# Optimization experiments

Measured on AMD Instinct MI355X. Metric: run time of the kernel, lower is better.

Reference implementation:

```python
import jax, jax.numpy as jnp
import numpy as np

B, S, DIM = 2, 2048, 2048
NH, NKV = 32, 8
HD = DIM // NH  # 64


def setup_inputs() -> dict:
    key = jax.random.key(0)
    ks = jax.random.split(key, 6)
    x = jax.random.normal(ks[0], (B, S, DIM), jnp.float32)
    # realistic rotary tables: [S, HD//2]
    inv_freq = 1.0 / (10000.0 ** (jnp.arange(0, HD, 2, dtype=jnp.float32) / HD))
    freqs = jnp.arange(S, dtype=jnp.float32)[:, None] * inv_freq[None, :]
    cos, sin = jnp.cos(freqs), jnp.sin(freqs)
    init = lambda k, shape: jax.random.normal(k, shape, jnp.float32) * (shape[0] ** -0.5)
    Wq = init(ks[1], (DIM, NH * HD))
    Wk = init(ks[2], (DIM, NKV * HD))
    Wv = init(ks[3], (DIM, NKV * HD))
    Wo = init(ks[4], (NH * HD, DIM))
    return {"x": x, "cos": cos, "sin": sin, "Wq": Wq, "Wk": Wk, "Wv": Wv, "Wo": Wo}


def _rope(t, c, s):
    # t: [B, S, H, HD]; c, s: [1, S, 1, HD//2]; consecutive-pair (v1) style
    b, sl, h, hd = t.shape
    tp = t.reshape(b, sl, h, hd // 2, 2)
    t0, t1 = tp[..., 0], tp[..., 1]
    return jnp.stack([t0 * c - t1 * s, t0 * s + t1 * c], axis=-1).reshape(b, sl, h, hd)


def reference(x, cos, sin, Wq, Wk, Wv, Wo):
    b, sl, _ = x.shape
    q = (x @ Wq).reshape(b, sl, NH, HD)
    k = (x @ Wk).reshape(b, sl, NKV, HD)
    v = (x @ Wv).reshape(b, sl, NKV, HD)
    c = cos[None, :, None, :]
    s = sin[None, :, None, :]
    q = _rope(q, c, s)
    k = _rope(k, c, s)
    n_rep = NH // NKV
    k = jnp.repeat(k, n_rep, axis=2)  # GQA repeat_interleave over heads
    v = jnp.repeat(v, n_rep, axis=2)
    scale = 1.0 / np.sqrt(HD)
    scores = jnp.einsum("bqhd,bkhd->bhqk", q, k) * scale  # [B, H, S, S]
    causal = jnp.tril(jnp.ones((sl, sl), dtype=bool))
    scores = jnp.where(causal[None, None], scores, -jnp.inf)
    p = jax.nn.softmax(scores, axis=-1)
    out = jnp.einsum("bhqk,bkhd->bqhd", p, v).reshape(b, sl, NH * HD)
    return out @ Wo
```

## Files before the change

### kernel.cpp

```cpp
#include <hip/hip_runtime.h>
#include <hip/hip_bf16.h>


typedef __attribute__((ext_vector_type(8))) short short8;
typedef __attribute__((ext_vector_type(4))) float f32x4;
typedef __attribute__((ext_vector_type(16))) float f32x16;
typedef __attribute__((ext_vector_type(2))) int i32x2;
typedef __attribute__((ext_vector_type(4))) int i32x4;

__device__ __forceinline__ unsigned short f2bfu(float f){
  unsigned u = __float_as_uint(f);
  u += 0x7FFFu + ((u >> 16) & 1u);
  return (unsigned short)(u >> 16);
}
__device__ __forceinline__ float bfu2f(unsigned short u){
  return __uint_as_float(((unsigned)u) << 16);
}
__device__ __forceinline__ unsigned cvt_pk_bf16(float lo, float hi){
  unsigned r;
  asm("v_cvt_pk_bf16_f32 %0, %1, %2" : "=v"(r) : "v"(lo), "v"(hi));
  return r;
}
__device__ __forceinline__ i32x2 pl32swap(int a, int b){
  auto r = __builtin_amdgcn_permlane32_swap(a, b, false, false);
  return __builtin_bit_cast(i32x2, r);
}
__device__ __forceinline__ int swz64(int row, int slot){
  return row * 64 + (((slot) ^ (row & 7)) << 3);
}
template<int N> __device__ __forceinline__ void vm_wait(){
  if constexpr (N == 8)      asm volatile("s_waitcnt vmcnt(8)" ::: "memory");
  else if constexpr (N == 7) asm volatile("s_waitcnt vmcnt(7)" ::: "memory");
  else if constexpr (N == 6) asm volatile("s_waitcnt vmcnt(6)" ::: "memory");
  else if constexpr (N == 4) asm volatile("s_waitcnt vmcnt(4)" ::: "memory");
  else if constexpr (N == 3) asm volatile("s_waitcnt vmcnt(3)" ::: "memory");
  else if constexpr (N == 2) asm volatile("s_waitcnt vmcnt(2)" ::: "memory");
  else                       asm volatile("s_waitcnt vmcnt(0)" ::: "memory");
}

__global__ void convx_kernel(const float* __restrict__ x, unsigned short* __restrict__ xb, int n4){
  int i = blockIdx.x * blockDim.x + threadIdx.x;
  if (i >= n4) return;
  float4 v = reinterpret_cast<const float4*>(x)[i];
  ushort4 o;
  o.x = f2bfu(v.x); o.y = f2bfu(v.y); o.z = f2bfu(v.z); o.w = f2bfu(v.w);
  reinterpret_cast<ushort4*>(xb)[i] = o;
}

__global__ void transpose_conv_kernel(const float* __restrict__ in, unsigned short* __restrict__ out,
                                      int Min, int Nin){
  __shared__ float t[32][33];
  int c0 = blockIdx.x * 32, r0 = blockIdx.y * 32;
  int tx = threadIdx.x, ty = threadIdx.y;
  #pragma unroll
  for (int i = ty; i < 32; i += 8) t[i][tx] = in[(size_t)(r0 + i) * Nin + c0 + tx];
  __syncthreads();
  #pragma unroll
  for (int i = ty; i < 32; i += 8) out[(size_t)(c0 + i) * Min + r0 + tx] = f2bfu(t[tx][i]);
}

#define PH4(SLOT,KK,VMW,...) { \
  const unsigned short* sAc = &sA[SLOT][(KK)*8192]; \
  const unsigned short* sBc = &sB[SLOT][(KK)*RB]; \
  short8 afr[8]; short8 bfr[4]; \
  _Pragma("unroll") for (int m_ = 0; m_ < 8; m_++) \
    afr[m_] = *reinterpret_cast<const short8*>(sAc + aOff[m_]); \
  _Pragma("unroll") for (int n_ = 0; n_ < NF; n_++) \
    bfr[n_] = *reinterpret_cast<const short8*>(sBc + bOff[n_]); \
  __VA_ARGS__; \
  __builtin_amdgcn_s_barrier(); \
  asm volatile("s_waitcnt lgkmcnt(0)" ::: "memory"); \
  __builtin_amdgcn_sched_barrier(0); \
  __builtin_amdgcn_s_setprio(1); \
  _Pragma("unroll") for (int m_ = 0; m_ < 8; m_++){ \
    _Pragma("unroll") for (int n_ = 0; n_ < NF; n_++){ \
      acc[m_][n_] = __builtin_amdgcn_mfma_f32_16x16x32_bf16(afr[m_], bfr[n_], acc[m_][n_], 0, 0, 0); }} \
  __builtin_amdgcn_s_setprio(0); \
  VMW; \
  __builtin_amdgcn_s_barrier(); \
}

template<int NF, bool OUTBF16>
__global__ __launch_bounds__(512, 2) void gemm4p_kernel(const unsigned short* __restrict__ A,
                                                        const unsigned short* __restrict__ B,
                                                        void* __restrict__ Cp,
                                                        int M, int N, int K, int nbx){
  constexpr int RB  = NF * 2048;
  constexpr int VMS = (NF == 4) ? 8 : (NF == 3 ? 7 : 6);
  __shared__ unsigned short sA[2][16384];
  __shared__ unsigned short sB[2][2 * RB];
  const int tid = threadIdx.x;
  const int l = tid & 63, w = tid >> 6;
  const int quad = l >> 4, c16 = l & 15;
  const int cpx = (int)gridDim.x >> 3;
  const int id2 = ((int)blockIdx.x & 7) * cpx + ((int)blockIdx.x >> 3);
  const int bx = id2 % nbx, by = id2 / nbx;
  const int row0 = by * 256, col0 = bx * (NF * 64);
  const int wr = w >> 2, wc = w & 3;

  const int rlA0 = w * 32 + (l >> 2), rlA1 = rlA0 + 16;
  const unsigned short* gA0 = A + (size_t)(row0 + rlA0) * K + (((l & 3) ^ ((rlA0 >> 1) & 3)) << 3);
  const unsigned short* gA1 = A + (size_t)(row0 + rlA1) * K + (((l & 3) ^ ((rlA1 >> 1) & 3)) << 3);
  const unsigned short* gB0;
  const unsigned short* gB1 = nullptr;
  const unsigned short* gB2 = nullptr;
  if constexpr (NF == 4){
    gB0 = B + (size_t)(col0 + rlA0) * K + (((l & 3) ^ ((rlA0 >> 1) & 3)) << 3);
    gB1 = B + (size_t)(col0 + rlA1) * K + (((l & 3) ^ ((rlA1 >> 1) & 3)) << 3);
  } else {
    const int rlB0 = w * 16 + (l >> 2);
    gB0 = B + (size_t)(col0 + rlB0) * K + (((l & 3) ^ ((rlB0 >> 1) & 3)) << 3);
    if constexpr (NF == 3){
      const int rlB2 = 128 + (w & 3) * 16 + (l >> 2);
      gB2 = B + (size_t)(col0 + rlB2) * K + (((l & 3) ^ ((rlB2 >> 1) & 3)) << 3);
    }
  }

  auto stA = [&](int slot, int kk, int col){
    __builtin_amdgcn_global_load_lds((const __attribute__((address_space(1))) void*)(gA0 + col),
        (__attribute__((address_space(3))) void*)(&sA[slot][kk * 8192 + w * 1024]), 16, 0, 0);
    __builtin_amdgcn_global_load_lds((const __attribute__((address_space(1))) void*)(gA1 + col),
        (__attribute__((address_space(3))) void*)(&sA[slot][kk * 8192 + w * 1024 + 512]), 16, 0, 0);
  };
  auto stB = [&](int slot, int kk, int col){
    if constexpr (NF == 4){
      __builtin_amdgcn_global_load_lds((const __attribute__((address_space(1))) void*)(gB0 + col),
          (__attribute__((address_space(3))) void*)(&sB[slot][kk * RB + w * 1024]), 16, 0, 0);
      __builtin_amdgcn_global_load_lds((const __attribute__((address_space(1))) void*)(gB1 + col),
          (__attribute__((address_space(3))) void*)(&sB[slot][kk * RB + w * 1024 + 512]), 16, 0, 0);
    } else if constexpr (NF == 3){
      __builtin_amdgcn_global_load_lds((const __attribute__((address_space(1))) void*)(gB0 + col),
          (__attribute__((address_space(3))) void*)(&sB[slot][kk * RB + w * 512]), 16, 0, 0);
      if ((kk == 0) ? (w < 4) : (w >= 4))
        __builtin_amdgcn_global_load_lds((const __attribute__((address_space(1))) void*)(gB2 + col),
            (__attribute__((address_space(3))) void*)(&sB[slot][kk * RB + 4096 + (w & 3) * 512]), 16, 0, 0);
    } else {
      __builtin_amdgcn_global_load_lds((const __attribute__((address_space(1))) void*)(gB0 + col),
          (__attribute__((address_space(3))) void*)(&sB[slot][kk * RB + w * 512]), 16, 0, 0);
    }
  };

  int aOff[8], bOff[4];
  #pragma unroll
  for (int mf = 0; mf < 8; mf++){
    int row = wr * 128 + mf * 16 + c16;
    aOff[mf] = row * 32 + ((quad ^ ((row >> 1) & 3)) << 3);
  }
  #pragma unroll
  for (int nf = 0; nf < 4; nf++){
    int row = wc * (NF * 16) + nf * 16 + c16;
    bOff[nf] = row * 32 + ((quad ^ ((row >> 1) & 3)) << 3);
  }

  stA(0, 0, 0);  stB(0, 0, 0);
  stA(0, 1, 32); stB(0, 1, 32);
  stA(1, 0, 64); stB(1, 0, 64);
  vm_wait<VMS>();
  __builtin_amdgcn_s_barrier();

  f32x4 acc[8][4] = {};
  const int NI = K >> 7;
  #pragma unroll 1
  for (int j = 0; j < NI - 1; ++j){
    const int t1c  = (2 * j + 1) * 64 + 32;
    const int t2c0 = (2 * j + 2) * 64;
    const int t2c1 = t2c0 + 32;
    const int t3c0 = (2 * j + 3) * 64;
    PH4(0,0, vm_wait<VMS>(), stA(1,1,t1c);  stB(1,1,t1c))
    PH4(0,1, vm_wait<VMS>(), stA(0,0,t2c0); stB(0,0,t2c0))
    PH4(1,0, vm_wait<VMS>(), stA(0,1,t2c1); stB(0,1,t2c1))
    PH4(1,1, vm_wait<VMS>(), stA(1,0,t3c0); stB(1,0,t3c0))
  }
  {
    const int t1c = K - 32;
    PH4(0,0, vm_wait<VMS>(), stA(1,1,t1c); stB(1,1,t1c))
    PH4(0,1, vm_wait<0>(), ;)
    PH4(1,0, vm_wait<0>(), ;)
    PH4(1,1, (void)0, ;)
  }

  #pragma unroll
  for (int mf = 0; mf < 8; mf++)
    #pragma unroll
    for (int nf = 0; nf < NF; nf++)
      #pragma unroll
      for (int r = 0; r < 4; r++){
        size_t off = (size_t)(row0 + wr * 128 + mf * 16 + quad * 4 + r) * N + (col0 + wc * (NF * 16) + nf * 16 + c16);
        if (OUTBF16) ((unsigned short*)Cp)[off] = f2bfu(acc[mf][nf][r]);
        else         ((float*)Cp)[off] = acc[mf][nf][r];
      }
}

__global__ void rope_kernel(const unsigned short* __restrict__ qkv, const float* __restrict__ cosb,
                            const float* __restrict__ sinb, unsigned short* __restrict__ Qo,
                            unsigned short* __restrict__ Ko){
  int idx = blockIdx.x * 256 + threadIdx.x;
  const int NQ = 4096 * 1024;
  if (idx < NQ){
    int m = idx >> 10, p = idx & 1023;
    int h = p >> 5, i = p & 31;
    int s = m & 2047;
    unsigned pr = *reinterpret_cast<const unsigned*>(qkv + (size_t)m * 3072 + h * 64 + 2 * i);
    float t0 = bfu2f((unsigned short)(pr & 0xFFFFu));
    float t1 = bfu2f((unsigned short)(pr >> 16));
    float c = cosb[s * 32 + i], sn = sinb[s * 32 + i];
    const float SC = 0.18033688011112042f;
    float o0 = (t0 * c - t1 * sn) * SC;
    float o1 = (t0 * sn + t1 * c) * SC;
    unsigned ow = (unsigned)f2bfu(o0) | ((unsigned)f2bfu(o1) << 16);
    *reinterpret_cast<unsigned*>(Qo + (size_t)m * 2048 + h * 64 + 2 * i) = ow;
  } else {
    int j = idx - NQ;
    int m = j >> 8, p = j & 255;
    int kvh = p >> 5, i = p & 31;
    int s = m & 2047, b = m >> 11;
    unsigned pr = *reinterpret_cast<const unsigned*>(qkv + (size_t)m * 3072 + 2048 + kvh * 64 + 2 * i);
    float t0 = bfu2f((unsigned short)(pr & 0xFFFFu));
    float t1 = bfu2f((unsigned short)(pr >> 16));
    float c = cosb[s * 32 + i], sn = sinb[s * 32 + i];
    float o0 = t0 * c - t1 * sn;
    float o1 = t0 * sn + t1 * c;
    unsigned ow = (unsigned)f2bfu(o0) | ((unsigned)f2bfu(o1) << 16);
    *reinterpret_cast<unsigned*>(Ko + ((size_t)(b * 8 + kvh) * 2048 + s) * 64 + 2 * i) = ow;
  }
}

__global__ void vtrans_kernel(const unsigned short* __restrict__ qkv, unsigned short* __restrict__ Vt){
  __shared__ float t[64][65];
  int bh = blockIdx.y;
  int s0 = blockIdx.x * 64;
  int b = bh >> 3, kvh = bh & 7;
  int tid = threadIdx.x;
  #pragma unroll
  for (int it = 0; it < 16; it++){
    int id = it * 256 + tid;
    int sl = id >> 6, d = id & 63;
    unsigned short u = qkv[(size_t)(b * 2048 + s0 + sl) * 3072 + 2560 + kvh * 64 + d];
    t[sl][d] = bfu2f(u);
  }
  __syncthreads();
  #pragma unroll
  for (int it = 0; it < 16; it++){
    int id = it * 256 + tid;
    int dl = id >> 6, sl = id & 63;
    Vt[((size_t)(b * 8 + kvh) * 64 + dl) * 2048 + s0 + sl] = f2bfu(t[sl][dl]);
  }
}

__global__ __launch_bounds__(256) void attn_kernel(const unsigned short* __restrict__ Q,
                                                   const unsigned short* __restrict__ Kt,
                                                   const unsigned short* __restrict__ Vt,
                                                   unsigned short* __restrict__ O){
  __shared__ unsigned short sK[2][64 * 64];
  __shared__ unsigned short sV[2][64 * 64];
  const int tid = threadIdx.x;
  const int l = tid & 63, w = tid >> 6;
  const int q32 = l & 31, hi = l >> 5;
  const int bid = blockIdx.x;
  const int qt = 15 - (bid >> 6);
  const int bh = bid & 63;
  const int b = bh >> 5, h = bh & 31, kvh = h >> 2;
  const int q0w = qt * 128 + w * 32;
  const int nt = 2 * qt + 2;

  const unsigned short* Kb = Kt + (size_t)(b * 8 + kvh) * 2048 * 64;
  const unsigned short* Vb = Vt + (size_t)(b * 8 + kvh) * 64 * 2048;

  auto stage = [&](int kv0, int buf){
    #pragma unroll
    for (int c = 0; c < 2; c++){
      const int rl = w * 16 + c * 8 + (l >> 3);
      const int ce = (((l & 7) ^ (l >> 3)) << 3);
      __builtin_amdgcn_global_load_lds(
        (const __attribute__((address_space(1))) void*)(Kb + (size_t)(kv0 + rl) * 64 + ce),
        (__attribute__((address_space(3))) void*)(&sK[buf][(w * 16 + c * 8) * 64]), 16, 0, 0);
      __builtin_amdgcn_global_load_lds(
        (const __attribute__((address_space(1))) void*)(Vb + (size_t)rl * 2048 + kv0 + ce),
        (__attribute__((address_space(3))) void*)(&sV[buf][(w * 16 + c * 8) * 64]), 16, 0, 0);
    }
  };

  short8 qv[4];
  {
    const unsigned short* Qp = Q + (size_t)(b * 2048 + q0w + q32) * 2048 + h * 64 + hi * 8;
    #pragma unroll
    for (int kd = 0; kd < 4; kd++) qv[kd] = *reinterpret_cast<const short8*>(Qp + kd * 16);
  }

  const short8 ones = {0x3F80, 0x3F80, 0x3F80, 0x3F80, 0x3F80, 0x3F80, 0x3F80, 0x3F80};

  f32x16 accA = {}, accB = {};
  f32x16 accl = {};

#define MKAP(Z, R0, AP) { \
    unsigned A_ = cvt_pk_bf16(Z[R0+0], Z[R0+1]); \
    unsigned B_ = cvt_pk_bf16(Z[R0+2], Z[R0+3]); \
    unsigned C_ = cvt_pk_bf16(Z[R0+4], Z[R0+5]); \
    unsigned D_ = cvt_pk_bf16(Z[R0+6], Z[R0+7]); \
    i32x2 s1_ = pl32swap((int)A_, (int)C_); \
    i32x2 s2_ = pl32swap((int)B_, (int)D_); \
    i32x4 q_ = {s1_[0], s2_[0], s1_[1], s2_[1]}; \
    AP = __builtin_bit_cast(short8, q_); \
  }

  stage(0, 0);
  vm_wait<0>();
  __builtin_amdgcn_s_barrier();

  for (int t = 0; t < nt; ++t){
    const int kv0 = t * 64;
    const int buf = t & 1;
    if (t + 1 < nt) stage((t + 1) * 64, buf ^ 1);

    const unsigned short* sKc = &sK[buf][0];
    const unsigned short* sVc = &sV[buf][0];

    f32x16 z0 = {}, z1 = {};
    __builtin_amdgcn_s_setprio(1);
    #pragma unroll
    for (int kd = 0; kd < 4; kd++){
      const int u = kd * 2 + hi;
      short8 ak0 = *reinterpret_cast<const short8*>(&sKc[swz64(q32, u)]);
      short8 ak1 = *reinterpret_cast<const short8*>(&sKc[swz64(32 + q32, u)]);
      z0 = __builtin_amdgcn_mfma_f32_32x32x16_bf16(ak0, qv[kd], z0, 0, 0, 0);
      z1 = __builtin_amdgcn_mfma_f32_32x32x16_bf16(ak1, qv[kd], z1, 0, 0, 0);
    }
    __builtin_amdgcn_s_setprio(0);

    if (kv0 + 63 > q0w){
      const int qg = q0w + q32;
      #pragma unroll
      for (int r = 0; r < 16; r++){
        const int kr = (r & 3) + 8 * (r >> 2) + 4 * hi;
        if (kv0 + kr > qg)      z0[r] = -1e30f;
        if (kv0 + 32 + kr > qg) z1[r] = -1e30f;
      }
    }

    #pragma unroll
    for (int r = 0; r < 16; r++){
      z0[r] = __builtin_amdgcn_exp2f(z0[r]);
      z1[r] = __builtin_amdgcn_exp2f(z1[r]);
    }

    short8 apA, apB;
    __builtin_amdgcn_s_setprio(1);
    MKAP(z0, 0, apA)
    MKAP(z0, 8, apB)
    accl = __builtin_amdgcn_mfma_f32_32x32x16_bf16(apA, ones, accl, 0, 0, 0);
    accl = __builtin_amdgcn_mfma_f32_32x32x16_bf16(apB, ones, accl, 0, 0, 0);
    {
      short8 bv;
      bv = *reinterpret_cast<const short8*>(&sVc[swz64(q32, 0 * 2 + hi)]);
      accA = __builtin_amdgcn_mfma_f32_32x32x16_bf16(apA, bv, accA, 0, 0, 0);
      bv = *reinterpret_cast<const short8*>(&sVc[swz64(q32, 1 * 2 + hi)]);
      accA = __builtin_amdgcn_mfma_f32_32x32x16_bf16(apB, bv, accA, 0, 0, 0);
      bv = *reinterpret_cast<const short8*>(&sVc[swz64(32 + q32, 0 * 2 + hi)]);
      accB = __builtin_amdgcn_mfma_f32_32x32x16_bf16(apA, bv, accB, 0, 0, 0);
      bv = *reinterpret_cast<const short8*>(&sVc[swz64(32 + q32, 1 * 2 + hi)]);
      accB = __builtin_amdgcn_mfma_f32_32x32x16_bf16(apB, bv, accB, 0, 0, 0);
    }
    MKAP(z1, 0, apA)
    MKAP(z1, 8, apB)
    accl = __builtin_amdgcn_mfma_f32_32x32x16_bf16(apA, ones, accl, 0, 0, 0);
    accl = __builtin_amdgcn_mfma_f32_32x32x16_bf16(apB, ones, accl, 0, 0, 0);
    {
      short8 bv;
      bv = *reinterpret_cast<const short8*>(&sVc[swz64(q32, 2 * 2 + hi)]);
      accA = __builtin_amdgcn_mfma_f32_32x32x16_bf16(apA, bv, accA, 0, 0, 0);
      bv = *reinterpret_cast<const short8*>(&sVc[swz64(q32, 3 * 2 + hi)]);
      accA = __builtin_amdgcn_mfma_f32_32x32x16_bf16(apB, bv, accA, 0, 0, 0);
      bv = *reinterpret_cast<const short8*>(&sVc[swz64(32 + q32, 2 * 2 + hi)]);
      accB = __builtin_amdgcn_mfma_f32_32x32x16_bf16(apA, bv, accB, 0, 0, 0);
      bv = *reinterpret_cast<const short8*>(&sVc[swz64(32 + q32, 3 * 2 + hi)]);
      accB = __builtin_amdgcn_mfma_f32_32x32x16_bf16(apB, bv, accB, 0, 0, 0);
    }
    __builtin_amdgcn_s_setprio(0);

    vm_wait<0>();
    __builtin_amdgcn_s_barrier();
  }
#undef MKAP

  #pragma unroll
  for (int r = 0; r < 16; r++){
    const float inv = 1.0f / accl[r];
    const int qrow = q0w + (r & 3) + 8 * (r >> 2) + 4 * hi;
    const size_t base = (size_t)(b * 2048 + qrow) * 2048 + h * 64 + q32;
    O[base]      = f2bfu(accA[r] * inv);
    O[base + 32] = f2bfu(accB[r] * inv);
  }
}

extern "C" void kernel_launch(void* const* d_in, const int* in_sizes, int n_in,
                              void* d_out, int out_size, void* d_ws, size_t ws_size,
                              hipStream_t stream){
  (void)in_sizes; (void)n_in; (void)out_size; (void)ws_size;
  const float* x  = (const float*)d_in[0];
  const float* cb = (const float*)d_in[1];
  const float* sb = (const float*)d_in[2];
  const float* Wq = (const float*)d_in[3];
  const float* Wk = (const float*)d_in[4];
  const float* Wv = (const float*)d_in[5];
  const float* Wo = (const float*)d_in[6];
  float* out = (float*)d_out;
  char* ws = (char*)d_ws;

  unsigned short* qkv = (unsigned short*)(ws + 0);
  unsigned short* xb  = (unsigned short*)(ws + 25165824);
  unsigned short* wt  = (unsigned short*)(ws + 41943040);
  unsigned short* qb  = (unsigned short*)(ws + 54525952);
  unsigned short* kb  = (unsigned short*)(ws + 71303168);
  unsigned short* vt  = (unsigned short*)(ws + 75497472);

  dim3 tb(32, 8);
  convx_kernel<<<8192, 256, 0, stream>>>(x, xb, 2097152);
  transpose_conv_kernel<<<dim3(64, 64), tb, 0, stream>>>(Wq, wt, 2048, 2048);
  transpose_conv_kernel<<<dim3(16, 64), tb, 0, stream>>>(Wk, wt + (size_t)2048 * 2048, 2048, 512);
  transpose_conv_kernel<<<dim3(16, 64), tb, 0, stream>>>(Wv, wt + (size_t)2560 * 2048, 2048, 512);
  gemm4p_kernel<3, true><<<256, 512, 0, stream>>>(xb, wt, qkv, 4096, 3072, 2048, 16);
  rope_kernel<<<20480, 256, 0, stream>>>(qkv, cb, sb, qb, kb);
  vtrans_kernel<<<dim3(32, 16), 256, 0, stream>>>(qkv, vt);
  transpose_conv_kernel<<<dim3(64, 64), tb, 0, stream>>>(Wo, wt, 2048, 2048);
  attn_kernel<<<1024, 256, 0, stream>>>(qb, kb, vt, xb);
  gemm4p_kernel<2, false><<<256, 512, 0, stream>>>(xb, wt, out, 4096, 2048, 2048, 16);
}
```

Baseline: 194.8 us.

## Double-buffer GEMM LDS fragments in registers to overlap reads with MFMA

The bf16 GEMM main loop now loads the next phase's A/B fragments from shared memory into a second register buffer while MFMAs run on the current fragments. This removes the pre-compute barrier and the LDS-latency stall at the start of each phase. A prologue preloads the first fragments and an epilogue macro handles the last compute. The global-load wait count is retuned for the new schedule. The second fragment buffer raises register pressure under the 512-thread, 2-block launch bounds, which risks spills or lower occupancy.

After: 196.0 us. No clear change (+0.6%).

```diff
diff --git a/kernel.cpp b/kernel.cpp
--- a/kernel.cpp
+++ b/kernel.cpp
@@ -59,25 +59,30 @@
   for (int i = ty; i < 32; i += 8) out[(size_t)(c0 + i) * Min + r0 + tx] = f2bfu(t[tx][i]);
 }
 
-#define PH4(SLOT,KK,VMW,...) { \
-  const unsigned short* sAc = &sA[SLOT][(KK)*8192]; \
-  const unsigned short* sBc = &sB[SLOT][(KK)*RB]; \
-  short8 afr[8]; short8 bfr[4]; \
+#define PH4P(NS,NK,CUR,NXT,VMW,...) { \
+  const unsigned short* sAn = &sA[NS][(NK)*8192]; \
+  const unsigned short* sBn = &sB[NS][(NK)*RB]; \
   _Pragma("unroll") for (int m_ = 0; m_ < 8; m_++) \
-    afr[m_] = *reinterpret_cast<const short8*>(sAc + aOff[m_]); \
+    afr[NXT][m_] = *reinterpret_cast<const short8*>(sAn + aOff[m_]); \
   _Pragma("unroll") for (int n_ = 0; n_ < NF; n_++) \
-    bfr[n_] = *reinterpret_cast<const short8*>(sBc + bOff[n_]); \
+    bfr[NXT][n_] = *reinterpret_cast<const short8*>(sBn + bOff[n_]); \
   __VA_ARGS__; \
-  __builtin_amdgcn_s_barrier(); \
-  asm volatile("s_waitcnt lgkmcnt(0)" ::: "memory"); \
   __builtin_amdgcn_sched_barrier(0); \
   __builtin_amdgcn_s_setprio(1); \
   _Pragma("unroll") for (int m_ = 0; m_ < 8; m_++){ \
     _Pragma("unroll") for (int n_ = 0; n_ < NF; n_++){ \
-      acc[m_][n_] = __builtin_amdgcn_mfma_f32_16x16x32_bf16(afr[m_], bfr[n_], acc[m_][n_], 0, 0, 0); }} \
+      acc[m_][n_] = __builtin_amdgcn_mfma_f32_16x16x32_bf16(afr[CUR][m_], bfr[CUR][n_], acc[m_][n_], 0, 0, 0); }} \
   __builtin_amdgcn_s_setprio(0); \
+  asm volatile("s_waitcnt lgkmcnt(0)" ::: "memory"); \
   VMW; \
   __builtin_amdgcn_s_barrier(); \
+}
+#define PH4L(CUR) { \
+  __builtin_amdgcn_s_setprio(1); \
+  _Pragma("unroll") for (int m_ = 0; m_ < 8; m_++){ \
+    _Pragma("unroll") for (int n_ = 0; n_ < NF; n_++){ \
+      acc[m_][n_] = __builtin_amdgcn_mfma_f32_16x16x32_bf16(afr[CUR][m_], bfr[CUR][n_], acc[m_][n_], 0, 0, 0); }} \
+  __builtin_amdgcn_s_setprio(0); \
 }
 
 template<int NF, bool OUTBF16>
@@ -85,8 +90,8 @@
                                                         const unsigned short* __restrict__ B,
                                                         void* __restrict__ Cp,
                                                         int M, int N, int K, int nbx){
-  constexpr int RB  = NF * 2048;
-  constexpr int VMS = (NF == 4) ? 8 : (NF == 3 ? 7 : 6);
+  constexpr int RB   = NF * 2048;
+  constexpr int VMS2 = (NF == 4) ? 4 : 3;
   __shared__ unsigned short sA[2][16384];
   __shared__ unsigned short sB[2][2 * RB];
   const int tid = threadIdx.x;
@@ -155,10 +160,17 @@
   stA(0, 0, 0);  stB(0, 0, 0);
   stA(0, 1, 32); stB(0, 1, 32);
   stA(1, 0, 64); stB(1, 0, 64);
-  vm_wait<VMS>();
+  vm_wait<VMS2>();
   __builtin_amdgcn_s_barrier();
 
   f32x4 acc[8][4] = {};
+  short8 afr[2][8];
+  short8 bfr[2][4];
+  #pragma unroll
+  for (int m_ = 0; m_ < 8; m_++) afr[0][m_] = *reinterpret_cast<const short8*>(&sA[0][0] + aOff[m_]);
+  #pragma unroll
+  for (int n_ = 0; n_ < NF; n_++) bfr[0][n_] = *reinterpret_cast<const short8*>(&sB[0][0] + bOff[n_]);
+
   const int NI = K >> 7;
   #pragma unroll 1
   for (int j = 0; j < NI - 1; ++j){
@@ -166,17 +178,17 @@
     const int t2c0 = (2 * j + 2) * 64;
     const int t2c1 = t2c0 + 32;
     const int t3c0 = (2 * j + 3) * 64;
-    PH4(0,0, vm_wait<VMS>(), stA(1,1,t1c);  stB(1,1,t1c))
-    PH4(0,1, vm_wait<VMS>(), stA(0,0,t2c0); stB(0,0,t2c0))
-    PH4(1,0, vm_wait<VMS>(), stA(0,1,t2c1); stB(0,1,t2c1))
-    PH4(1,1, vm_wait<VMS>(), stA(1,0,t3c0); stB(1,0,t3c0))
+    PH4P(0,1, 0,1, vm_wait<VMS2>(), stA(1,1,t1c);  stB(1,1,t1c))
+    PH4P(1,0, 1,0, vm_wait<VMS2>(), stA(0,0,t2c0); stB(0,0,t2c0))
+    PH4P(1,1, 0,1, vm_wait<VMS2>(), stA(0,1,t2c1); stB(0,1,t2c1))
+    PH4P(0,0, 1,0, vm_wait<VMS2>(), stA(1,0,t3c0); stB(1,0,t3c0))
   }
   {
     const int t1c = K - 32;
-    PH4(0,0, vm_wait<VMS>(), stA(1,1,t1c); stB(1,1,t1c))
-    PH4(0,1, vm_wait<0>(), ;)
-    PH4(1,0, vm_wait<0>(), ;)
-    PH4(1,1, (void)0, ;)
+    PH4P(0,1, 0,1, vm_wait<VMS2>(), stA(1,1,t1c); stB(1,1,t1c))
+    PH4P(1,0, 1,0, vm_wait<0>(), ;)
+    PH4P(1,1, 0,1, (void)0, ;)
+    PH4L(1)
   }
 
   #pragma unroll
```

## Retile GEMM to 128-row blocks with 4 waves and larger per-wave N tiles

Applied to the files above, without the earlier changes.

Shrinks the GEMM block tile from 256 rows with 8 waves to 128 rows with 4 waves (2x2 wave grid), each wave computing 64 rows by 2*NF*16 columns. The grid doubles to 512 blocks, which changes wave quantisation across CUs, and LDS use per block drops. The global-to-LDS load mapping is generalised and the vmcnt thresholds are rescaled to match. Each block now loads more B data relative to its A tile, which lowers arithmetic intensity per block.

Measured after the change: 193.3 us. About the same (-0.8%).

```diff
diff --git a/kernel.cpp b/kernel.cpp
--- a/kernel.cpp
+++ b/kernel.cpp
@@ -29,13 +29,15 @@
   return row * 64 + (((slot) ^ (row & 7)) << 3);
 }
 template<int N> __device__ __forceinline__ void vm_wait(){
-  if constexpr (N == 8)      asm volatile("s_waitcnt vmcnt(8)" ::: "memory");
-  else if constexpr (N == 7) asm volatile("s_waitcnt vmcnt(7)" ::: "memory");
-  else if constexpr (N == 6) asm volatile("s_waitcnt vmcnt(6)" ::: "memory");
-  else if constexpr (N == 4) asm volatile("s_waitcnt vmcnt(4)" ::: "memory");
-  else if constexpr (N == 3) asm volatile("s_waitcnt vmcnt(3)" ::: "memory");
-  else if constexpr (N == 2) asm volatile("s_waitcnt vmcnt(2)" ::: "memory");
-  else                       asm volatile("s_waitcnt vmcnt(0)" ::: "memory");
+  if constexpr (N == 10)      asm volatile("s_waitcnt vmcnt(10)" ::: "memory");
+  else if constexpr (N == 8)  asm volatile("s_waitcnt vmcnt(8)" ::: "memory");
+  else if constexpr (N == 7)  asm volatile("s_waitcnt vmcnt(7)" ::: "memory");
+  else if constexpr (N == 6)  asm volatile("s_waitcnt vmcnt(6)" ::: "memory");
+  else if constexpr (N == 5)  asm volatile("s_waitcnt vmcnt(5)" ::: "memory");
+  else if constexpr (N == 4)  asm volatile("s_waitcnt vmcnt(4)" ::: "memory");
+  else if constexpr (N == 3)  asm volatile("s_waitcnt vmcnt(3)" ::: "memory");
+  else if constexpr (N == 2)  asm volatile("s_waitcnt vmcnt(2)" ::: "memory");
+  else                        asm volatile("s_waitcnt vmcnt(0)" ::: "memory");
 }
 
 __global__ void convx_kernel(const float* __restrict__ x, unsigned short* __restrict__ xb, int n4){
@@ -60,20 +62,20 @@
 }
 
 #define PH4(SLOT,KK,VMW,...) { \
-  const unsigned short* sAc = &sA[SLOT][(KK)*8192]; \
+  const unsigned short* sAc = &sA[SLOT][(KK)*4096]; \
   const unsigned short* sBc = &sB[SLOT][(KK)*RB]; \
-  short8 afr[8]; short8 bfr[4]; \
-  _Pragma("unroll") for (int m_ = 0; m_ < 8; m_++) \
+  short8 afr[4]; short8 bfr[6]; \
+  _Pragma("unroll") for (int m_ = 0; m_ < 4; m_++) \
     afr[m_] = *reinterpret_cast<const short8*>(sAc + aOff[m_]); \
-  _Pragma("unroll") for (int n_ = 0; n_ < NF; n_++) \
+  _Pragma("unroll") for (int n_ = 0; n_ < NFR; n_++) \
     bfr[n_] = *reinterpret_cast<const short8*>(sBc + bOff[n_]); \
   __VA_ARGS__; \
   __builtin_amdgcn_s_barrier(); \
   asm volatile("s_waitcnt lgkmcnt(0)" ::: "memory"); \
   __builtin_amdgcn_sched_barrier(0); \
   __builtin_amdgcn_s_setprio(1); \
-  _Pragma("unroll") for (int m_ = 0; m_ < 8; m_++){ \
-    _Pragma("unroll") for (int n_ = 0; n_ < NF; n_++){ \
+  _Pragma("unroll") for (int m_ = 0; m_ < 4; m_++){ \
+    _Pragma("unroll") for (int n_ = 0; n_ < NFR; n_++){ \
       acc[m_][n_] = __builtin_amdgcn_mfma_f32_16x16x32_bf16(afr[m_], bfr[n_], acc[m_][n_], 0, 0, 0); }} \
   __builtin_amdgcn_s_setprio(0); \
   VMW; \
@@ -81,13 +83,14 @@
 }
 
 template<int NF, bool OUTBF16>
-__global__ __launch_bounds__(512, 2) void gemm4p_kernel(const unsigned short* __restrict__ A,
+__global__ __launch_bounds__(256, 2) void gemm4p_kernel(const unsigned short* __restrict__ A,
                                                         const unsigned short* __restrict__ B,
                                                         void* __restrict__ Cp,
                                                         int M, int N, int K, int nbx){
+  constexpr int NFR = 2 * NF;
   constexpr int RB  = NF * 2048;
-  constexpr int VMS = (NF == 4) ? 8 : (NF == 3 ? 7 : 6);
-  __shared__ unsigned short sA[2][16384];
+  constexpr int VMS = 2 * (2 + NF);
+  __shared__ unsigned short sA[2][8192];
   __shared__ unsigned short sB[2][2 * RB];
   const int tid = threadIdx.x;
   const int l = tid & 63, w = tid >> 6;
@@ -95,60 +98,44 @@
   const int cpx = (int)gridDim.x >> 3;
   const int id2 = ((int)blockIdx.x & 7) * cpx + ((int)blockIdx.x >> 3);
   const int bx = id2 % nbx, by = id2 / nbx;
-  const int row0 = by * 256, col0 = bx * (NF * 64);
-  const int wr = w >> 2, wc = w & 3;
-
-  const int rlA0 = w * 32 + (l >> 2), rlA1 = rlA0 + 16;
-  const unsigned short* gA0 = A + (size_t)(row0 + rlA0) * K + (((l & 3) ^ ((rlA0 >> 1) & 3)) << 3);
-  const unsigned short* gA1 = A + (size_t)(row0 + rlA1) * K + (((l & 3) ^ ((rlA1 >> 1) & 3)) << 3);
-  const unsigned short* gB0;
-  const unsigned short* gB1 = nullptr;
-  const unsigned short* gB2 = nullptr;
-  if constexpr (NF == 4){
-    gB0 = B + (size_t)(col0 + rlA0) * K + (((l & 3) ^ ((rlA0 >> 1) & 3)) << 3);
-    gB1 = B + (size_t)(col0 + rlA1) * K + (((l & 3) ^ ((rlA1 >> 1) & 3)) << 3);
-  } else {
-    const int rlB0 = w * 16 + (l >> 2);
-    gB0 = B + (size_t)(col0 + rlB0) * K + (((l & 3) ^ ((rlB0 >> 1) & 3)) << 3);
-    if constexpr (NF == 3){
-      const int rlB2 = 128 + (w & 3) * 16 + (l >> 2);
-      gB2 = B + (size_t)(col0 + rlB2) * K + (((l & 3) ^ ((rlB2 >> 1) & 3)) << 3);
-    }
+  const int row0 = by * 128, col0 = bx * (NF * 64);
+  const int wr = w >> 1, wc = w & 1;
+
+  const unsigned short* gAp[2];
+  const unsigned short* gBp[NF];
+  #pragma unroll
+  for (int j = 0; j < 2; j++){
+    int rl = w * 32 + j * 16 + (l >> 2);
+    gAp[j] = A + (size_t)(row0 + rl) * K + ((((l & 3) ^ ((rl >> 1) & 3))) << 3);
+  }
+  #pragma unroll
+  for (int j = 0; j < NF; j++){
+    int rl = w * (16 * NF) + j * 16 + (l >> 2);
+    gBp[j] = B + (size_t)(col0 + rl) * K + ((((l & 3) ^ ((rl >> 1) & 3))) << 3);
   }
 
   auto stA = [&](int slot, int kk, int col){
-    __builtin_amdgcn_global_load_lds((const __attribute__((address_space(1))) void*)(gA0 + col),
-        (__attribute__((address_space(3))) void*)(&sA[slot][kk * 8192 + w * 1024]), 16, 0, 0);
-    __builtin_amdgcn_global_load_lds((const __attribute__((address_space(1))) void*)(gA1 + col),
-        (__attribute__((address_space(3))) void*)(&sA[slot][kk * 8192 + w * 1024 + 512]), 16, 0, 0);
+    #pragma unroll
+    for (int j = 0; j < 2; j++)
+      __builtin_amdgcn_global_load_lds((const __attribute__((address_space(1))) void*)(gAp[j] + col),
+          (__attribute__((address_space(3))) void*)(&sA[slot][kk * 4096 + w * 1024 + j * 512]), 16, 0, 0);
   };
   auto stB = [&](int slot, int kk, int col){
-    if constexpr (NF == 4){
-      __builtin_amdgcn_global_load_lds((const __attribute__((address_space(1))) void*)(gB0 + col),
-          (__attribute__((address_space(3))) void*)(&sB[slot][kk * RB + w * 1024]), 16, 0, 0);
-      __builtin_amdgcn_global_load_lds((const __attribute__((address_space(1))) void*)(gB1 + col),
-          (__attribute__((address_space(3))) void*)(&sB[slot][kk * RB + w * 1024 + 512]), 16, 0, 0);
-    } else if constexpr (NF == 3){
-      __builtin_amdgcn_global_load_lds((const __attribute__((address_space(1))) void*)(gB0 + col),
-          (__attribute__((address_space(3))) void*)(&sB[slot][kk * RB + w * 512]), 16, 0, 0);
-      if ((kk == 0) ? (w < 4) : (w >= 4))
-        __builtin_amdgcn_global_load_lds((const __attribute__((address_space(1))) void*)(gB2 + col),
-            (__attribute__((address_space(3))) void*)(&sB[slot][kk * RB + 4096 + (w & 3) * 512]), 16, 0, 0);
-    } else {
-      __builtin_amdgcn_global_load_lds((const __attribute__((address_space(1))) void*)(gB0 + col),
-          (__attribute__((address_space(3))) void*)(&sB[slot][kk * RB + w * 512]), 16, 0, 0);
-    }
+    #pragma unroll
+    for (int j = 0; j < NF; j++)
+      __builtin_amdgcn_global_load_lds((const __attribute__((address_space(1))) void*)(gBp[j] + col),
+          (__attribute__((address_space(3))) void*)(&sB[slot][kk * RB + w * (512 * NF) + j * 512]), 16, 0, 0);
   };
 
-  int aOff[8], bOff[4];
-  #pragma unroll
-  for (int mf = 0; mf < 8; mf++){
-    int row = wr * 128 + mf * 16 + c16;
+  int aOff[4], bOff[6];
+  #pragma unroll
+  for (int mf = 0; mf < 4; mf++){
+    int row = wr * 64 + mf * 16 + c16;
     aOff[mf] = row * 32 + ((quad ^ ((row >> 1) & 3)) << 3);
   }
   #pragma unroll
-  for (int nf = 0; nf < 4; nf++){
-    int row = wc * (NF * 16) + nf * 16 + c16;
+  for (int nf = 0; nf < NFR; nf++){
+    int row = wc * (NF * 32) + nf * 16 + c16;
     bOff[nf] = row * 32 + ((quad ^ ((row >> 1) & 3)) << 3);
   }
 
@@ -158,7 +145,7 @@
   vm_wait<VMS>();
   __builtin_amdgcn_s_barrier();
 
-  f32x4 acc[8][4] = {};
+  f32x4 acc[4][6] = {};
   const int NI = K >> 7;
   #pragma unroll 1
   for (int j = 0; j < NI - 1; ++j){
@@ -180,12 +167,12 @@
   }
 
   #pragma unroll
-  for (int mf = 0; mf < 8; mf++)
-    #pragma unroll
-    for (int nf = 0; nf < NF; nf++)
+  for (int mf = 0; mf < 4; mf++)
+    #pragma unroll
+    for (int nf = 0; nf < NFR; nf++)
       #pragma unroll
       for (int r = 0; r < 4; r++){
-        size_t off = (size_t)(row0 + wr * 128 + mf * 16 + quad * 4 + r) * N + (col0 + wc * (NF * 16) + nf * 16 + c16);
+        size_t off = (size_t)(row0 + wr * 64 + mf * 16 + quad * 4 + r) * N + (col0 + wc * (NF * 32) + nf * 16 + c16);
         if (OUTBF16) ((unsigned short*)Cp)[off] = f2bfu(acc[mf][nf][r]);
         else         ((float*)Cp)[off] = acc[mf][nf][r];
       }
@@ -418,10 +405,10 @@
   transpose_conv_kernel<<<dim3(64, 64), tb, 0, stream>>>(Wq, wt, 2048, 2048);
   transpose_conv_kernel<<<dim3(16, 64), tb, 0, stream>>>(Wk, wt + (size_t)2048 * 2048, 2048, 512);
   transpose_conv_kernel<<<dim3(16, 64), tb, 0, stream>>>(Wv, wt + (size_t)2560 * 2048, 2048, 512);
-  gemm4p_kernel<3, true><<<256, 512, 0, stream>>>(xb, wt, qkv, 4096, 3072, 2048, 16);
+  gemm4p_kernel<3, true><<<512, 256, 0, stream>>>(xb, wt, qkv, 4096, 3072, 2048, 16);
   rope_kernel<<<20480, 256, 0, stream>>>(qkv, cb, sb, qb, kb);
   vtrans_kernel<<<dim3(32, 16), 256, 0, stream>>>(qkv, vt);
   transpose_conv_kernel<<<dim3(64, 64), tb, 0, stream>>>(Wo, wt, 2048, 2048);
   attn_kernel<<<1024, 256, 0, stream>>>(qb, kb, vt, xb);
-  gemm4p_kernel<2, false><<<256, 512, 0, stream>>>(xb, wt, out, 4096, 2048, 2048, 16);
-}
+  gemm4p_kernel<2, false><<<512, 256, 0, stream>>>(xb, wt, out, 4096, 2048, 2048, 16);
+}
```
